# Optimization experiments

Measured on AMD Instinct MI355X. Metric: run time of the kernel, lower is better.

The kernel has to match this reference:

```python
import jax, jax.numpy as jnp
import numpy as np

B, N, E = 4, 1024, 8192
NF_IN, NF_H, NF_OUT = 32, 128, 3


def _lin(key, fan_in, fan_out):
    k1, k2 = jax.random.split(key)
    bound = 1.0 / np.sqrt(fan_in)
    W = jax.random.uniform(k1, (fan_in, fan_out), jnp.float32, -bound, bound)
    b = jax.random.uniform(k2, (fan_out,), jnp.float32, -bound, bound)
    return W, b


def setup_inputs() -> dict:
    key = jax.random.key(0)
    ks = jax.random.split(key, 16)
    x = jax.random.normal(ks[0], (B, N, NF_IN), jnp.float32)
    # One-hot receiver/sender relation matrices [B, E, N]
    recv = jax.random.randint(ks[1], (B, E), 0, N)
    send = jax.random.randint(ks[2], (B, E), 0, N)
    Rr = jax.nn.one_hot(recv, N, dtype=jnp.float32)
    Rs = jax.nn.one_hot(send, N, dtype=jnp.float32)
    neW0, neb0 = _lin(ks[3], NF_IN, NF_H)
    neW1, neb1 = _lin(ks[4], NF_H, NF_H)
    neW2, neb2 = _lin(ks[5], NF_H, NF_H)
    eeW0, eeb0 = _lin(ks[6], NF_IN * 2, NF_H)
    eeW1, eeb1 = _lin(ks[7], NF_H, NF_H)
    eeW2, eeb2 = _lin(ks[8], NF_H, NF_H)
    npW, npb = _lin(ks[9], NF_H * 2, NF_H)
    epW, epb = _lin(ks[10], NF_H * 3, NF_H)
    ppW0, ppb0 = _lin(ks[11], NF_H * 2, NF_H)
    ppW1, ppb1 = _lin(ks[12], NF_H, NF_H)
    ppW2, ppb2 = _lin(ks[13], NF_H, NF_OUT)
    return dict(x=x, Rr=Rr, Rs=Rs, pstep=2,
                neW0=neW0, neb0=neb0, neW1=neW1, neb1=neb1, neW2=neW2, neb2=neb2,
                eeW0=eeW0, eeb0=eeb0, eeW1=eeW1, eeb1=eeb1, eeW2=eeW2, eeb2=eeb2,
                npW=npW, npb=npb, epW=epW, epb=epb,
                ppW0=ppW0, ppb0=ppb0, ppW1=ppW1, ppb1=ppb1, ppW2=ppW2, ppb2=ppb2)


def _encoder(x, W0, b0, W1, b1, W2, b2):
    # Linear->ReLU x3 (ReLU after last layer too)
    h = jax.nn.relu(x @ W0 + b0)
    h = jax.nn.relu(h @ W1 + b1)
    return jax.nn.relu(h @ W2 + b2)


def _predictor(x, W0, b0, W1, b1, W2, b2):
    h = jax.nn.relu(x @ W0 + b0)
    h = jax.nn.relu(h @ W1 + b1)
    return h @ W2 + b2


def reference(x, Rr, Rs, pstep,
              neW0, neb0, neW1, neb1, neW2, neb2,
              eeW0, eeb0, eeW1, eeb1, eeW2, eeb2,
              npW, npb, epW, epb,
              ppW0, ppb0, ppW1, ppb1, ppW2, ppb2):
    node_encode = _encoder(x, neW0, neb0, neW1, neb1, neW2, neb2)  # [B,N,H]
    node_effect = node_encode
    x_r = jnp.einsum('ben,bnf->bef', Rr, x)  # gather receiver features
    x_s = jnp.einsum('ben,bnf->bef', Rs, x)  # gather sender features
    edge_encode = _encoder(jnp.concatenate([x_r, x_s], -1),
                           eeW0, eeb0, eeW1, eeb1, eeW2, eeb2)  # [B,E,H]
    for _ in range(pstep):
        ne_r = jnp.einsum('ben,bnh->beh', Rr, node_effect)
        ne_s = jnp.einsum('ben,bnh->beh', Rs, node_effect)
        edge_in = jnp.concatenate([edge_encode, ne_r, ne_s], -1)  # [B,E,3H]
        edge_effect = jax.nn.relu(edge_in @ epW + epb)  # [B,E,H]
        agg = jnp.einsum('ben,beh->bnh', Rr, edge_effect)  # scatter-add to receivers
        node_in = jnp.concatenate([node_encode, agg], -1)  # [B,N,2H]
        node_effect = jax.nn.relu(node_in @ npW + npb + node_effect)  # residual
    node_reps = _predictor(jnp.concatenate([node_encode, node_effect], -1),
                           ppW0, ppb0, ppW1, ppb1, ppW2, ppb2)  # [B,N,out]
    return node_reps
```

## Files before the change

kernel.cpp:

```cpp
#include <hip/hip_runtime.h>
#include <hip/hip_bf16.h>


typedef unsigned short u16;
typedef __attribute__((ext_vector_type(8))) __bf16 bf16x8;
typedef __attribute__((ext_vector_type(4))) float f32x4;

#define N_    1024
#define BN    4096
#define BE    32768
#define LOG_E 13
#define H_    128
#define LSTR  132
#define ECAP  64
#define ASTR  136

__device__ __forceinline__ u16 f2bf(float f) {
    __bf16 h = (__bf16)f;
    return __builtin_bit_cast(u16, h);
}

__device__ __forceinline__ bf16x8 cvt8(float4 f0, float4 f1) {
    bf16x8 a;
    a[0] = (__bf16)f0.x; a[1] = (__bf16)f0.y; a[2] = (__bf16)f0.z; a[3] = (__bf16)f0.w;
    a[4] = (__bf16)f1.x; a[5] = (__bf16)f1.y; a[6] = (__bf16)f1.z; a[7] = (__bf16)f1.w;
    return a;
}

__device__ __forceinline__ bf16x8 a_from_f32(const float* p) {
    float4 f0 = *(const float4*)p;
    float4 f1 = *(const float4*)(p + 4);
    return cvt8(f0, f1);
}

__device__ __forceinline__ bf16x8 a_from_lds(const float* lds, int r, int quad, int c) {
    return a_from_f32(lds + r * LSTR + c * 32 + quad * 8);
}

__device__ __forceinline__ void mm8L(const u16* wb, int cc, bf16x8 a,
                                     f32x4* acc, int lane) {
    const u16* wp = wb + cc * 4096;
    #pragma unroll
    for (int nt = 0; nt < 8; ++nt) {
        bf16x8 bw = *(const bf16x8*)(wp + (nt * 64 + lane) * 8);
        acc[nt] = __builtin_amdgcn_mfma_f32_16x16x32_bf16(a, bw, acc[nt], 0, 0, 0);
    }
}

__device__ __forceinline__ void mm2(const u16* __restrict__ Wf, int c, int ntb,
                                    bf16x8 a, f32x4* acc, int lane) {
    const u16* wp = Wf + ((size_t)c * 8) * 64 * 8;
    #pragma unroll
    for (int nt = 0; nt < 2; ++nt) {
        bf16x8 bw = *(const bf16x8*)(wp + (size_t)((ntb + nt) * 64 + lane) * 8);
        acc[nt] = __builtin_amdgcn_mfma_f32_16x16x32_bf16(a, bw, acc[nt], 0, 0, 0);
    }
}

__device__ __forceinline__ void zacc8(f32x4* acc) {
    #pragma unroll
    for (int t = 0; t < 8; ++t) acc[t] = (f32x4){0.f, 0.f, 0.f, 0.f};
}
__device__ __forceinline__ void zacc2(f32x4* acc) {
    acc[0] = (f32x4){0.f, 0.f, 0.f, 0.f};
    acc[1] = (f32x4){0.f, 0.f, 0.f, 0.f};
}

__device__ __forceinline__ void stage_w(u16* dst, const u16* __restrict__ src,
                                        int n16, int tid) {
    for (int t = tid; t < n16; t += 256)
        *(bf16x8*)(dst + t * 8) = *(const bf16x8*)(src + t * 8);
}

__device__ __forceinline__ void epi8_bf(u16* t, const f32x4* acc,
                                        const float* __restrict__ bias,
                                        int quad, int m) {
    #pragma unroll
    for (int nt = 0; nt < 8; ++nt) {
        float bv = bias[nt * 16 + m];
        #pragma unroll
        for (int i = 0; i < 4; ++i)
            t[(quad * 4 + i) * ASTR + nt * 16 + m] =
                f2bf(fmaxf(acc[nt][i] + bv, 0.f));
    }
}

__device__ __forceinline__ void epi2_lds(float* lds, const f32x4* acc,
                                         const float* __restrict__ bias,
                                         int quad, int m, int ntb) {
    #pragma unroll
    for (int nt = 0; nt < 2; ++nt) {
        int col = (ntb + nt) * 16 + m;
        float bv = bias[col];
        #pragma unroll
        for (int i = 0; i < 4; ++i)
            lds[(quad * 4 + i) * LSTR + col] = fmaxf(acc[nt][i] + bv, 0.f);
    }
}

struct WDesc { const float* src; u16* dst; int K; };
struct WPack { WDesc d[10]; };

__global__ __launch_bounds__(256) void k_prep(WPack P,
                                              const float* __restrict__ Rr,
                                              const float* __restrict__ Rs,
                                              int* __restrict__ recv,
                                              int* __restrict__ send,
                                              int* __restrict__ deg,
                                              int* __restrict__ eidx) {
    int bx = blockIdx.x;
    if (bx >= 16384) {
        int t = bx - 16384;
        WDesc d = P.d[t / 192];
        int i = (t % 192) * 256 + threadIdx.x;
        if (i >= d.K * 128) return;
        int j    = i & 7;
        int lane = (i >> 3) & 63;
        int nt   = (i >> 9) & 7;
        int c    = i >> 12;
        int k = c * 32 + (lane >> 4) * 8 + j;
        int n = nt * 16 + (lane & 15);
        d.dst[i] = f2bf(d.src[k * 128 + n]);
        return;
    }
    int wave = threadIdx.x >> 6, lane = threadIdx.x & 63;
    int g = bx * 4 + wave;
    const float* src;
    int* dst;
    if (g < BE) { src = Rr + (size_t)g * N_;        dst = recv + g; }
    else        { src = Rs + (size_t)(g - BE) * N_; dst = send + (g - BE); }
    int idx = 0;
    bool done = false;
    #pragma unroll
    for (int it = 0; it < 4; ++it) {
        if (!done) {
            int base = it * 256 + lane * 4;
            float4 v = *(const float4*)(src + base);
            int found = -1;
            if      (v.x != 0.f) found = base;
            else if (v.y != 0.f) found = base + 1;
            else if (v.z != 0.f) found = base + 2;
            else if (v.w != 0.f) found = base + 3;
            unsigned long long msk = __ballot(found >= 0);
            if (msk) {
                int sl = __ffsll((long long)msk) - 1;
                idx = __shfl(found, sl, 64);
                done = true;
            }
        }
    }
    if (lane == 0) {
        *dst = idx;
        if (g < BE) {
            int node = (g >> LOG_E) * N_ + idx;
            int pos = atomicAdd(deg + node, 1);
            if (pos < ECAP) eidx[node * ECAP + pos] = g;
        }
    }
}

__global__ __launch_bounds__(256) void k_enc(
    const float* __restrict__ x,
    const int* __restrict__ recv, const int* __restrict__ send,
    const u16* __restrict__ nW0, const float* __restrict__ nb0,
    const u16* __restrict__ nW1, const float* __restrict__ nb1,
    const u16* __restrict__ nW2, const float* __restrict__ nb2,
    const u16* __restrict__ eW0, const float* __restrict__ eb0,
    const u16* __restrict__ eW1, const float* __restrict__ eb1,
    const u16* __restrict__ eW2, const float* __restrict__ eb2,
    float* __restrict__ nenc_f, u16* __restrict__ nenc_bf,
    u16* __restrict__ eenc)
{
    __shared__ union U {
        struct { u16 wbuf[8192]; u16 tile[4][2][16 * ASTR]; } e;
        struct { float lds[2][16 * LSTR]; } n;
    } sm;
    int tid = threadIdx.x, lane = tid & 63, w = tid >> 6;
    int m = lane & 15, quad = lane >> 4;

    if (blockIdx.x < 512) {
        int myrow16 = blockIdx.x * 64 + w * 16;
        int e = myrow16 + m, b = e >> LOG_E;
        long rr = (long)b * N_ + recv[e];
        long rs = (long)b * N_ + send[e];
        u16* t0 = sm.e.tile[w][0];
        u16* t1 = sm.e.tile[w][1];
        f32x4 acc[8];

        stage_w(sm.e.wbuf, eW0, 1024, tid);
        __syncthreads();
        zacc8(acc);
        mm8L(sm.e.wbuf, 0, a_from_f32(x + rr * 32 + quad * 8), acc, lane);
        mm8L(sm.e.wbuf, 1, a_from_f32(x + rs * 32 + quad * 8), acc, lane);
        epi8_bf(t0, acc, eb0, quad, m);
        __syncthreads();

        zacc8(acc);
        #pragma unroll
        for (int h = 0; h < 2; ++h) {
            stage_w(sm.e.wbuf, eW1 + h * 8192, 1024, tid);
            __syncthreads();
            #pragma unroll
            for (int cp = 0; cp < 2; ++cp) {
                int c = h * 2 + cp;
                bf16x8 a = *(const bf16x8*)(t0 + m * ASTR + c * 32 + quad * 8);
                mm8L(sm.e.wbuf, cp, a, acc, lane);
            }
            __syncthreads();
        }
        epi8_bf(t1, acc, eb1, quad, m);

        zacc8(acc);
        #pragma unroll
        for (int h = 0; h < 2; ++h) {
            stage_w(sm.e.wbuf, eW2 + h * 8192, 1024, tid);
            __syncthreads();
            #pragma unroll
            for (int cp = 0; cp < 2; ++cp) {
                int c = h * 2 + cp;
                bf16x8 a = *(const bf16x8*)(t1 + m * ASTR + c * 32 + quad * 8);
                mm8L(sm.e.wbuf, cp, a, acc, lane);
            }
            __syncthreads();
        }
        epi8_bf(t0, acc, eb2, quad, m);

        #pragma unroll
        for (int t = 0; t < 16; ++t)
            *(unsigned*)(eenc + (size_t)(myrow16 + t) * H_ + lane * 2) =
                *(const unsigned*)(t0 + t * ASTR + lane * 2);
        return;
    }

    int row16 = (blockIdx.x - 512) * 16, ntb = w * 2;
    f32x4 acc[2];

    zacc2(acc);
    mm2(nW0, 0, ntb, a_from_f32(x + (size_t)(row16 + m) * 32 + quad * 8), acc, lane);
    epi2_lds(sm.n.lds[0], acc, nb0, quad, m, ntb);
    __syncthreads();

    zacc2(acc);
    #pragma unroll
    for (int c = 0; c < 4; ++c)
        mm2(nW1, c, ntb, a_from_lds(sm.n.lds[0], m, quad, c), acc, lane);
    epi2_lds(sm.n.lds[1], acc, nb1, quad, m, ntb);
    __syncthreads();

    zacc2(acc);
    #pragma unroll
    for (int c = 0; c < 4; ++c)
        mm2(nW2, c, ntb, a_from_lds(sm.n.lds[1], m, quad, c), acc, lane);
    epi2_lds(sm.n.lds[0], acc, nb2, quad, m, ntb);
    __syncthreads();

    #pragma unroll
    for (int t = 0; t < 8; ++t) {
        int flat = t * 256 + tid, r = flat >> 7, col = flat & 127;
        nenc_f[(size_t)(row16 + r) * H_ + col] = sm.n.lds[0][r * LSTR + col];
    }
    #pragma unroll
    for (int t = 0; t < 4; ++t) {
        int p = t * 256 + tid, r = p >> 6, c2 = (p & 63) * 2;
        u16 lo = f2bf(sm.n.lds[0][r * LSTR + c2]);
        u16 hi = f2bf(sm.n.lds[0][r * LSTR + c2 + 1]);
        *(unsigned*)(nenc_bf + (size_t)(row16 + r) * H_ + c2) =
            (unsigned)lo | ((unsigned)hi << 16);
    }
}

__global__ __launch_bounds__(256) void k_eprop(
    const u16* __restrict__ eenc, const u16* __restrict__ eff_bf,
    const int* __restrict__ recv, const int* __restrict__ send,
    const u16* __restrict__ Wf, const float* __restrict__ bias,
    float* __restrict__ edge_eff)
{
    __shared__ u16 wbuf[16384];
    int tid = threadIdx.x, lane = tid & 63, w = tid >> 6;
    int m = lane & 15, quad = lane >> 4;
    int myrow16 = blockIdx.x * 64 + w * 16;
    int e = myrow16 + m;
    long rr = ((long)(e >> LOG_E) * N_ + recv[e]) * H_;
    long rs = ((long)(e >> LOG_E) * N_ + send[e]) * H_;
    f32x4 acc[8];
    zacc8(acc);

    #pragma unroll
    for (int g = 0; g < 3; ++g) {
        stage_w(wbuf, Wf + g * 16384, 2048, tid);
        __syncthreads();
        const u16* abase = (g == 0) ? eenc + (size_t)e * H_
                         : (g == 1) ? eff_bf + rr
                                    : eff_bf + rs;
        #pragma unroll
        for (int c = 0; c < 4; ++c) {
            bf16x8 a = *(const bf16x8*)(abase + c * 32 + quad * 8);
            mm8L(wbuf, c, a, acc, lane);
        }
        __syncthreads();
    }

    #pragma unroll
    for (int nt = 0; nt < 8; ++nt) {
        int col = nt * 16 + m;
        float bv = bias[col];
        #pragma unroll
        for (int i = 0; i < 4; ++i)
            edge_eff[(size_t)(myrow16 + quad * 4 + i) * H_ + col] =
                fmaxf(acc[nt][i] + bv, 0.f);
    }
}

__device__ __forceinline__ void gather_agg(u16* aggl, int row16, int tid, int lane,
                                           const float* __restrict__ edge_eff,
                                           const int* __restrict__ deg,
                                           const int* __restrict__ eidx) {
    int nd = tid >> 4, l = tid & 15;
    int node = row16 + nd;
    int dg = deg[node]; dg = dg < ECAP ? dg : ECAP;
    int ev = eidx[node * ECAP + l];
    int base = lane & 48;
    float s[8] = {0.f, 0.f, 0.f, 0.f, 0.f, 0.f, 0.f, 0.f};
    int d16 = dg < 16 ? dg : 16;
    int t = 0;
    for (; t + 1 < d16; t += 2) {
        int e0 = __shfl(ev, base | t, 64);
        int e1 = __shfl(ev, base | (t + 1), 64);
        const float* p0 = edge_eff + (size_t)e0 * H_ + l * 8;
        const float* p1 = edge_eff + (size_t)e1 * H_ + l * 8;
        float4 a0 = *(const float4*)p0, b0 = *(const float4*)(p0 + 4);
        float4 a1 = *(const float4*)p1, b1 = *(const float4*)(p1 + 4);
        s[0] += a0.x + a1.x; s[1] += a0.y + a1.y;
        s[2] += a0.z + a1.z; s[3] += a0.w + a1.w;
        s[4] += b0.x + b1.x; s[5] += b0.y + b1.y;
        s[6] += b0.z + b1.z; s[7] += b0.w + b1.w;
    }
    if (t < d16) {
        int e0 = __shfl(ev, base | t, 64);
        const float* p0 = edge_eff + (size_t)e0 * H_ + l * 8;
        float4 a0 = *(const float4*)p0, b0 = *(const float4*)(p0 + 4);
        s[0] += a0.x; s[1] += a0.y; s[2] += a0.z; s[3] += a0.w;
        s[4] += b0.x; s[5] += b0.y; s[6] += b0.z; s[7] += b0.w;
        ++t;
    }
    for (; t < dg; ++t) {
        int e0 = eidx[node * ECAP + t];
        const float* p0 = edge_eff + (size_t)e0 * H_ + l * 8;
        float4 a0 = *(const float4*)p0, b0 = *(const float4*)(p0 + 4);
        s[0] += a0.x; s[1] += a0.y; s[2] += a0.z; s[3] += a0.w;
        s[4] += b0.x; s[5] += b0.y; s[6] += b0.z; s[7] += b0.w;
    }
    bf16x8 o;
    #pragma unroll
    for (int j = 0; j < 8; ++j) o[j] = (__bf16)s[j];
    *(bf16x8*)(aggl + nd * ASTR + l * 8) = o;
}

__global__ __launch_bounds__(256) void k_nprop(
    const u16* __restrict__ nenc_bf, const float* __restrict__ edge_eff,
    const int* __restrict__ deg, const int* __restrict__ eidx,
    const float* __restrict__ eff_f,
    const u16* __restrict__ Wf, const float* __restrict__ bias,
    float* __restrict__ nout_f, u16* __restrict__ nout_bf)
{
    __shared__ u16 aggl[16 * ASTR];
    int tid = threadIdx.x, lane = tid & 63, w = tid >> 6;
    int m = lane & 15, quad = lane >> 4;
    int row16 = blockIdx.x * 16;

    gather_agg(aggl, row16, tid, lane, edge_eff, deg, eidx);
    __syncthreads();

    int row = row16 + m, ntb = w * 2;
    f32x4 acc[2];
    zacc2(acc);
    #pragma unroll
    for (int c = 0; c < 4; ++c)
        mm2(Wf, c, ntb,
            *(const bf16x8*)(nenc_bf + (size_t)row * H_ + c * 32 + quad * 8), acc, lane);
    #pragma unroll
    for (int c = 0; c < 4; ++c)
        mm2(Wf, 4 + c, ntb,
            *(const bf16x8*)(aggl + m * ASTR + c * 32 + quad * 8), acc, lane);

    #pragma unroll
    for (int nt = 0; nt < 2; ++nt) {
        int col = (ntb + nt) * 16 + m;
        float bv = bias[col];
        #pragma unroll
        for (int i = 0; i < 4; ++i) {
            int r = row16 + quad * 4 + i;
            float v = fmaxf(acc[nt][i] + bv + eff_f[(size_t)r * H_ + col], 0.f);
            nout_f[(size_t)r * H_ + col] = v;
            nout_bf[(size_t)r * H_ + col] = f2bf(v);
        }
    }
}

__global__ __launch_bounds__(256) void k_npropred(
    const u16* __restrict__ nenc_bf, const float* __restrict__ edge_eff,
    const int* __restrict__ deg, const int* __restrict__ eidx,
    const float* __restrict__ eff_f,
    const u16* __restrict__ Wnp, const float* __restrict__ bnp,
    const u16* __restrict__ Wp0, const float* __restrict__ bp0,
    const u16* __restrict__ Wp1, const float* __restrict__ bp1,
    const float* __restrict__ W2, const float* __restrict__ b2,
    float* __restrict__ out)
{
    __shared__ u16 aggl[16 * ASTR];
    __shared__ u16 vl[16 * ASTR];
    __shared__ u16 h1[16 * ASTR];
    __shared__ float h2[16 * LSTR];
    int tid = threadIdx.x, lane = tid & 63, w = tid >> 6;
    int m = lane & 15, quad = lane >> 4;
    int row16 = blockIdx.x * 16;

    gather_agg(aggl, row16, tid, lane, edge_eff, deg, eidx);
    __syncthreads();

    int row = row16 + m, ntb = w * 2;
    f32x4 acc[2];

    zacc2(acc);
    #pragma unroll
    for (int c = 0; c < 4; ++c)
        mm2(Wnp, c, ntb,
            *(const bf16x8*)(nenc_bf + (size_t)row * H_ + c * 32 + quad * 8), acc, lane);
    #pragma unroll
    for (int c = 0; c < 4; ++c)
        mm2(Wnp, 4 + c, ntb,
            *(const bf16x8*)(aggl + m * ASTR + c * 32 + quad * 8), acc, lane);
    #pragma unroll
    for (int nt = 0; nt < 2; ++nt) {
        int col = (ntb + nt) * 16 + m;
        float bv = bnp[col];
        #pragma unroll
        for (int i = 0; i < 4; ++i) {
            int r = quad * 4 + i;
            float v = fmaxf(acc[nt][i] + bv + eff_f[(size_t)(row16 + r) * H_ + col], 0.f);
            vl[r * ASTR + col] = f2bf(v);
        }
    }
    __syncthreads();

    zacc2(acc);
    #pragma unroll
    for (int c = 0; c < 4; ++c)
        mm2(Wp0, c, ntb,
            *(const bf16x8*)(nenc_bf + (size_t)row * H_ + c * 32 + quad * 8), acc, lane);
    #pragma unroll
    for (int c = 0; c < 4; ++c)
        mm2(Wp0, 4 + c, ntb,
            *(const bf16x8*)(vl + m * ASTR + c * 32 + quad * 8), acc, lane);
    #pragma unroll
    for (int nt = 0; nt < 2; ++nt) {
        int col = (ntb + nt) * 16 + m;
        float bv = bp0[col];
        #pragma unroll
        for (int i = 0; i < 4; ++i)
            h1[(quad * 4 + i) * ASTR + col] = f2bf(fmaxf(acc[nt][i] + bv, 0.f));
    }
    __syncthreads();

    zacc2(acc);
    #pragma unroll
    for (int c = 0; c < 4; ++c)
        mm2(Wp1, c, ntb,
            *(const bf16x8*)(h1 + m * ASTR + c * 32 + quad * 8), acc, lane);
    #pragma unroll
    for (int nt = 0; nt < 2; ++nt) {
        int col = (ntb + nt) * 16 + m;
        float bv = bp1[col];
        #pragma unroll
        for (int i = 0; i < 4; ++i)
            h2[(quad * 4 + i) * LSTR + col] = fmaxf(acc[nt][i] + bv, 0.f);
    }
    __syncthreads();

    if (w == 0) {
        int r = lane & 15, col = lane >> 4;
        if (col < 3) {
            float s = 0.f;
            #pragma unroll 8
            for (int k = 0; k < 128; ++k)
                s += h2[r * LSTR + k] * W2[k * 3 + col];
            out[(size_t)(row16 + r) * 3 + col] = s + b2[col];
        }
    }
}

extern "C" void kernel_launch(void* const* d_in, const int* in_sizes, int n_in,
                              void* d_out, int out_size, void* d_ws, size_t ws_size,
                              hipStream_t stream) {
    (void)in_sizes; (void)n_in; (void)out_size; (void)ws_size;

    const float* x    = (const float*)d_in[0];
    const float* Rr   = (const float*)d_in[1];
    const float* Rs   = (const float*)d_in[2];
    const float* neW0 = (const float*)d_in[4];  const float* neb0 = (const float*)d_in[5];
    const float* neW1 = (const float*)d_in[6];  const float* neb1 = (const float*)d_in[7];
    const float* neW2 = (const float*)d_in[8];  const float* neb2 = (const float*)d_in[9];
    const float* eeW0 = (const float*)d_in[10]; const float* eeb0 = (const float*)d_in[11];
    const float* eeW1 = (const float*)d_in[12]; const float* eeb1 = (const float*)d_in[13];
    const float* eeW2 = (const float*)d_in[14]; const float* eeb2 = (const float*)d_in[15];
    const float* npW  = (const float*)d_in[16]; const float* npb  = (const float*)d_in[17];
    const float* epW  = (const float*)d_in[18]; const float* epb  = (const float*)d_in[19];
    const float* ppW0 = (const float*)d_in[20]; const float* ppb0 = (const float*)d_in[21];
    const float* ppW1 = (const float*)d_in[22]; const float* ppb1 = (const float*)d_in[23];
    const float* ppW2 = (const float*)d_in[24]; const float* ppb2 = (const float*)d_in[25];

    char* ws = (char*)d_ws;
    size_t off = 0;
    auto alloc = [&](size_t bytes) -> char* {
        char* p = ws + off;
        off += (bytes + 255) & ~(size_t)255;
        return p;
    };

    u16* f_neW0 = (u16*)alloc(32  * 128 * 2);
    u16* f_neW1 = (u16*)alloc(128 * 128 * 2);
    u16* f_neW2 = (u16*)alloc(128 * 128 * 2);
    u16* f_eeW0 = (u16*)alloc(64  * 128 * 2);
    u16* f_eeW1 = (u16*)alloc(128 * 128 * 2);
    u16* f_eeW2 = (u16*)alloc(128 * 128 * 2);
    u16* f_epW  = (u16*)alloc(384 * 128 * 2);
    u16* f_npW  = (u16*)alloc(256 * 128 * 2);
    u16* f_ppW0 = (u16*)alloc(256 * 128 * 2);
    u16* f_ppW1 = (u16*)alloc(128 * 128 * 2);
    int*   recv = (int*)alloc(BE * 4);
    int*   send = (int*)alloc(BE * 4);
    int*   deg  = (int*)alloc(BN * 4);
    int*   eidx = (int*)alloc((size_t)BN * ECAP * 4);
    float* nenc_f  = (float*)alloc((size_t)BN * H_ * 4);
    u16*   nenc_bf = (u16*)alloc((size_t)BN * H_ * 2);
    float* nef1_f  = (float*)alloc((size_t)BN * H_ * 4);
    u16*   nef1_bf = (u16*)alloc((size_t)BN * H_ * 2);
    float* edge_eff = (float*)alloc((size_t)BE * H_ * 4);
    u16*   eenc = (u16*)alloc((size_t)BE * H_ * 2);

    WPack P;
    P.d[0] = {neW0, f_neW0, 32};
    P.d[1] = {neW1, f_neW1, 128};
    P.d[2] = {neW2, f_neW2, 128};
    P.d[3] = {eeW0, f_eeW0, 64};
    P.d[4] = {eeW1, f_eeW1, 128};
    P.d[5] = {eeW2, f_eeW2, 128};
    P.d[6] = {epW,  f_epW,  384};
    P.d[7] = {npW,  f_npW,  256};
    P.d[8] = {ppW0, f_ppW0, 256};
    P.d[9] = {ppW1, f_ppW1, 128};

    hipMemsetAsync(deg, 0, BN * 4, stream);

    k_prep<<<16384 + 1920, 256, 0, stream>>>(P, Rr, Rs, recv, send, deg, eidx);

    k_enc<<<512 + 256, 256, 0, stream>>>(x, recv, send,
                                         f_neW0, neb0, f_neW1, neb1, f_neW2, neb2,
                                         f_eeW0, eeb0, f_eeW1, eeb1, f_eeW2, eeb2,
                                         nenc_f, nenc_bf, eenc);

    k_eprop<<<BE / 64, 256, 0, stream>>>(eenc, nenc_bf, recv, send, f_epW, epb, edge_eff);
    k_nprop<<<BN / 16, 256, 0, stream>>>(nenc_bf, edge_eff, deg, eidx, nenc_f,
                                         f_npW, npb, nef1_f, nef1_bf);
    k_eprop<<<BE / 64, 256, 0, stream>>>(eenc, nef1_bf, recv, send, f_epW, epb, edge_eff);
    k_npropred<<<BN / 16, 256, 0, stream>>>(nenc_bf, edge_eff, deg, eidx, nef1_f,
                                            f_npW, npb, f_ppW0, ppb0, f_ppW1, ppb1,
                                            ppW2, ppb2, (float*)d_out);
}
```

Measured before the change: 365.4 us.

## Double-buffer LDS weight staging in edge encoder and edge propagation kernels

The edge-encoder and edge-propagation kernels now keep two LDS weight buffers. Each next weight chunk is staged while MFMAs run on the current one, which removes one barrier per chunk. In the propagation kernel, all gathered A-fragments (edge encoding plus receiver and sender node effects) are loaded into registers up front, so global gather latency overlaps with weight staging. The cost is a larger LDS footprint (64 KB in k_eprop) and more registers, which can lower occupancy.

```diff
diff --git a/kernel.cpp b/kernel.cpp
--- a/kernel.cpp
+++ b/kernel.cpp
@@ -172,7 +172,7 @@
     u16* __restrict__ eenc)
 {
     __shared__ union U {
-        struct { u16 wbuf[8192]; u16 tile[4][2][16 * ASTR]; } e;
+        struct { u16 wb[2][8192]; u16 tile[4][2][16 * ASTR]; } e;
         struct { float lds[2][16 * LSTR]; } n;
     } sm;
     int tid = threadIdx.x, lane = tid & 63, w = tid >> 6;
@@ -187,42 +187,39 @@
         u16* t1 = sm.e.tile[w][1];
         f32x4 acc[8];
 
-        stage_w(sm.e.wbuf, eW0, 1024, tid);
+        bf16x8 a_rr = a_from_f32(x + rr * 32 + quad * 8);
+        bf16x8 a_rs = a_from_f32(x + rs * 32 + quad * 8);
+
+        stage_w(sm.e.wb[0], eW0, 1024, tid);
         __syncthreads();
+
+        stage_w(sm.e.wb[1], eW1, 1024, tid);
         zacc8(acc);
-        mm8L(sm.e.wbuf, 0, a_from_f32(x + rr * 32 + quad * 8), acc, lane);
-        mm8L(sm.e.wbuf, 1, a_from_f32(x + rs * 32 + quad * 8), acc, lane);
+        mm8L(sm.e.wb[0], 0, a_rr, acc, lane);
+        mm8L(sm.e.wb[0], 1, a_rs, acc, lane);
         epi8_bf(t0, acc, eb0, quad, m);
         __syncthreads();
 
+        stage_w(sm.e.wb[0], eW1 + 8192, 1024, tid);
         zacc8(acc);
-        #pragma unroll
-        for (int h = 0; h < 2; ++h) {
-            stage_w(sm.e.wbuf, eW1 + h * 8192, 1024, tid);
-            __syncthreads();
-            #pragma unroll
-            for (int cp = 0; cp < 2; ++cp) {
-                int c = h * 2 + cp;
-                bf16x8 a = *(const bf16x8*)(t0 + m * ASTR + c * 32 + quad * 8);
-                mm8L(sm.e.wbuf, cp, a, acc, lane);
-            }
-            __syncthreads();
-        }
+        mm8L(sm.e.wb[1], 0, *(const bf16x8*)(t0 + m * ASTR + 0 * 32 + quad * 8), acc, lane);
+        mm8L(sm.e.wb[1], 1, *(const bf16x8*)(t0 + m * ASTR + 1 * 32 + quad * 8), acc, lane);
+        __syncthreads();
+
+        stage_w(sm.e.wb[1], eW2, 1024, tid);
+        mm8L(sm.e.wb[0], 0, *(const bf16x8*)(t0 + m * ASTR + 2 * 32 + quad * 8), acc, lane);
+        mm8L(sm.e.wb[0], 1, *(const bf16x8*)(t0 + m * ASTR + 3 * 32 + quad * 8), acc, lane);
         epi8_bf(t1, acc, eb1, quad, m);
-
+        __syncthreads();
+
+        stage_w(sm.e.wb[0], eW2 + 8192, 1024, tid);
         zacc8(acc);
-        #pragma unroll
-        for (int h = 0; h < 2; ++h) {
-            stage_w(sm.e.wbuf, eW2 + h * 8192, 1024, tid);
-            __syncthreads();
-            #pragma unroll
-            for (int cp = 0; cp < 2; ++cp) {
-                int c = h * 2 + cp;
-                bf16x8 a = *(const bf16x8*)(t1 + m * ASTR + c * 32 + quad * 8);
-                mm8L(sm.e.wbuf, cp, a, acc, lane);
-            }
-            __syncthreads();
-        }
+        mm8L(sm.e.wb[1], 0, *(const bf16x8*)(t1 + m * ASTR + 0 * 32 + quad * 8), acc, lane);
+        mm8L(sm.e.wb[1], 1, *(const bf16x8*)(t1 + m * ASTR + 1 * 32 + quad * 8), acc, lane);
+        __syncthreads();
+
+        mm8L(sm.e.wb[0], 0, *(const bf16x8*)(t1 + m * ASTR + 2 * 32 + quad * 8), acc, lane);
+        mm8L(sm.e.wb[0], 1, *(const bf16x8*)(t1 + m * ASTR + 3 * 32 + quad * 8), acc, lane);
         epi8_bf(t0, acc, eb2, quad, m);
 
         #pragma unroll
@@ -275,28 +272,33 @@
     const u16* __restrict__ Wf, const float* __restrict__ bias,
     float* __restrict__ edge_eff)
 {
-    __shared__ u16 wbuf[16384];
+    __shared__ u16 wbuf[2][16384];
     int tid = threadIdx.x, lane = tid & 63, w = tid >> 6;
     int m = lane & 15, quad = lane >> 4;
     int myrow16 = blockIdx.x * 64 + w * 16;
     int e = myrow16 + m;
     long rr = ((long)(e >> LOG_E) * N_ + recv[e]) * H_;
     long rs = ((long)(e >> LOG_E) * N_ + send[e]) * H_;
+
+    bf16x8 af[12];
+    #pragma unroll
+    for (int c = 0; c < 4; ++c) {
+        af[c]     = *(const bf16x8*)(eenc + (size_t)e * H_ + c * 32 + quad * 8);
+        af[4 + c] = *(const bf16x8*)(eff_bf + rr + c * 32 + quad * 8);
+        af[8 + c] = *(const bf16x8*)(eff_bf + rs + c * 32 + quad * 8);
+    }
+
     f32x4 acc[8];
     zacc8(acc);
 
+    stage_w(wbuf[0], Wf, 2048, tid);
+    __syncthreads();
     #pragma unroll
     for (int g = 0; g < 3; ++g) {
-        stage_w(wbuf, Wf + g * 16384, 2048, tid);
-        __syncthreads();
-        const u16* abase = (g == 0) ? eenc + (size_t)e * H_
-                         : (g == 1) ? eff_bf + rr
-                                    : eff_bf + rs;
-        #pragma unroll
-        for (int c = 0; c < 4; ++c) {
-            bf16x8 a = *(const bf16x8*)(abase + c * 32 + quad * 8);
-            mm8L(wbuf, c, a, acc, lane);
-        }
+        if (g < 2) stage_w(wbuf[(g + 1) & 1], Wf + (g + 1) * 16384, 2048, tid);
+        #pragma unroll
+        for (int c = 0; c < 4; ++c)
+            mm8L(wbuf[g & 1], c, af[g * 4 + c], acc, lane);
         __syncthreads();
     }
 
```

Measured after the change: 367.2 us. About the same (+0.5%).
